# Kernel optimization log

Hardware: AMD Instinct MI355X
Metric: run time of the kernel (lower is better)

Reference implementation:

```python
import jax, jax.numpy as jnp
import numpy as np

B, S, E, H, D = 2, 2048, 1024, 16, 64  # batch, seq(=max_seq_len), embed_dim, heads, atten_dim


def setup_inputs() -> dict:
    key = jax.random.key(0)
    ks = jax.random.split(key, 9)
    s = 0.02
    return {
        "x": jax.random.normal(ks[0], (B, S, E), jnp.float32),
        "Wq": jax.random.normal(ks[1], (H, E, D), jnp.float32) * s,
        "Wk": jax.random.normal(ks[2], (H, E, D), jnp.float32) * s,
        "Wv": jax.random.normal(ks[3], (H, E, D), jnp.float32) * s,
        "bq": jax.random.normal(ks[4], (H, D), jnp.float32) * s,
        "bk": jax.random.normal(ks[5], (H, D), jnp.float32) * s,
        "bv": jax.random.normal(ks[6], (H, D), jnp.float32) * s,
        "Wp": jax.random.normal(ks[7], (H * D, E), jnp.float32) * s,
        "bp": jax.random.normal(ks[8], (E,), jnp.float32) * s,
    }


def reference(x, Wq, Wk, Wv, bq, bk, bv, Wp, bp):
    scale = jnp.sqrt(jnp.float32(D))
    # per-head projections, all heads at once: [B,H,S,D]
    q = jnp.einsum("bse,hed->bhsd", x, Wq) + bq[:, None, :]
    k = jnp.einsum("bse,hed->bhsd", x, Wk) + bk[:, None, :]
    v = jnp.einsum("bse,hed->bhsd", x, Wv) + bv[:, None, :]
    # causal scores [B,H,S,S], additive -inf mask above diagonal (as in the buffer)
    score = jnp.einsum("bhsd,bhtd->bhst", q, k) / scale
    mask = jnp.triu(jnp.full((S, S), -jnp.inf, jnp.float32), k=1)
    score = score + mask
    probs = jax.nn.softmax(score, axis=-1)
    attn = jnp.einsum("bhst,bhtd->bhsd", probs, v)
    # concat heads -> [B,S,H*D], then projection + ReLU
    concat = attn.transpose(0, 2, 1, 3).reshape(B, S, H * D)
    out = jax.nn.relu(concat @ Wp + bp)
    return out
```

## Files before the change

kernel.cpp:

```cpp
#include <hip/hip_runtime.h>

#define S_LEN 2048
#define E_DIM 1024
#define H_NUM 16
#define D_DIM 64

typedef unsigned short u16;
using bf16x8 = __attribute__((ext_vector_type(8))) short;
using f32x4  = __attribute__((ext_vector_type(4))) float;

#define MFMA16(A, B, C) __builtin_amdgcn_mfma_f32_16x16x32_bf16(A, B, C, 0, 0, 0)

__device__ __forceinline__ u16 f2bf(float f) {
    unsigned u = __float_as_uint(f);
    u += 0x7fffu + ((u >> 16) & 1u);
    return (u16)(u >> 16);
}
__device__ __forceinline__ unsigned pack_bf16_tr(float lo, float hi) {
    return (__float_as_uint(lo) >> 16) | (__float_as_uint(hi) & 0xffff0000u);
}
__device__ __forceinline__ float bfu(unsigned u) { return __uint_as_float(u << 16); }
__device__ __forceinline__ f32x4 fzero4() { f32x4 z; z[0]=0.f; z[1]=0.f; z[2]=0.f; z[3]=0.f; return z; }

__device__ __forceinline__ void gll16(const u16* g, u16* l) {
    __builtin_amdgcn_global_load_lds(
        (const __attribute__((address_space(1))) void*)g,
        (__attribute__((address_space(3))) void*)l, 16, 0, 0);
}

__global__ __launch_bounds__(256) void cvt_bf16(const float* __restrict__ in, u16* __restrict__ outp, int n) {
    int i4 = (blockIdx.x * 256 + threadIdx.x) * 4;
    if (i4 < n) {
        float4 f = *(const float4*)(in + i4);
        unsigned lo = (unsigned)f2bf(f.x) | ((unsigned)f2bf(f.y) << 16);
        unsigned hi = (unsigned)f2bf(f.z) | ((unsigned)f2bf(f.w) << 16);
        uint2 p; p.x = lo; p.y = hi;
        *(uint2*)(outp + i4) = p;
    }
}

__device__ __forceinline__ void cvt_t_tile(const float* __restrict__ bin, u16* __restrict__ bout,
                                           int R, int C, int r0, int c0) {
    __shared__ float t[64][65];
    const int tid = threadIdx.x;
    const int lr = tid >> 2, lc = (tid & 3) * 16;

    const float* src = bin + (size_t)(r0 + lr) * C + c0 + lc;
    #pragma unroll
    for (int j = 0; j < 4; j++) {
        float4 f = *(const float4*)(src + j * 4);
        t[lr][lc + j * 4 + 0] = f.x; t[lr][lc + j * 4 + 1] = f.y;
        t[lr][lc + j * 4 + 2] = f.z; t[lr][lc + j * 4 + 3] = f.w;
    }
    __syncthreads();

    u16* dst = bout + (size_t)(c0 + lr) * R + r0 + lc;
    u16 vals[16];
    #pragma unroll
    for (int i = 0; i < 16; i++) vals[i] = f2bf(t[lc + i][lr]);
    uint4 pa, pb;
    pa.x = vals[0] | (vals[1] << 16);  pa.y = vals[2] | (vals[3] << 16);
    pa.z = vals[4] | (vals[5] << 16);  pa.w = vals[6] | (vals[7] << 16);
    pb.x = vals[8] | (vals[9] << 16);  pb.y = vals[10] | (vals[11] << 16);
    pb.z = vals[12] | (vals[13] << 16); pb.w = vals[14] | (vals[15] << 16);
    *(uint4*)dst = pa;
    *(uint4*)(dst + 8) = pb;
}

__global__ __launch_bounds__(256) void cvt_bf16_t(const float* __restrict__ in, u16* __restrict__ outp,
                                                  int R, int C) {
    const float* bin = in + (size_t)blockIdx.z * R * C;
    u16* bout = outp + (size_t)blockIdx.z * R * C;
    cvt_t_tile(bin, bout, R, C, blockIdx.y * 64, blockIdx.x * 64);
}

__global__ __launch_bounds__(256) void cvt_w3_t(
    const float* __restrict__ Wq, const float* __restrict__ Wk, const float* __restrict__ Wv,
    u16* __restrict__ wqt, u16* __restrict__ wkt, u16* __restrict__ wvt) {
    const int which = blockIdx.z >> 4, bh = blockIdx.z & 15;
    const float* in = (which == 0) ? Wq : (which == 1) ? Wk : Wv;
    u16* outp = (which == 0) ? wqt : (which == 1) ? wkt : wvt;
    const float* bin = in + (size_t)bh * E_DIM * D_DIM;
    u16* bout = outp + (size_t)bh * E_DIM * D_DIM;
    cvt_t_tile(bin, bout, E_DIM, D_DIM, blockIdx.y * 64, 0);
}

__global__ __launch_bounds__(256) void vt_prep(const u16* __restrict__ v, u16* __restrict__ vt) {
    const int st = blockIdx.x;
    const int bhi = blockIdx.y;
    __shared__ u16 t[64 * 72];
    const int tid = threadIdx.x;
    const int wave = tid >> 6, lane = tid & 63;

    const u16* src = v + (size_t)bhi * S_LEN * D_DIM + (size_t)(st * 64 + lane) * D_DIM + wave * 16;
    uint4 a = *(const uint4*)(src);
    uint4 b = *(const uint4*)(src + 8);
    unsigned w[8] = { a.x, a.y, a.z, a.w, b.x, b.y, b.z, b.w };
    #pragma unroll
    for (int j = 0; j < 8; j++) {
        t[(wave * 16 + 2 * j    ) * 72 + lane] = (u16)(w[j] & 0xffffu);
        t[(wave * 16 + 2 * j + 1) * 72 + lane] = (u16)(w[j] >> 16);
    }
    __syncthreads();

    const int dr = tid >> 2, sc = (tid & 3) * 16;
    u16* dst = vt + (size_t)bhi * D_DIM * S_LEN + (size_t)dr * S_LEN + st * 64 + sc;
    *(uint4*)(dst    ) = *(const uint4*)(&t[dr * 72 + sc    ]);
    *(uint4*)(dst + 8) = *(const uint4*)(&t[dr * 72 + sc + 8]);
}

__global__ __launch_bounds__(256) void qkv_gemm(
    const u16* __restrict__ xb, const u16* __restrict__ wcat,
    const float* __restrict__ bq, const float* __restrict__ bk, const float* __restrict__ bv,
    u16* __restrict__ oq, u16* __restrict__ okk, u16* __restrict__ ov)
{
    const int m0 = blockIdx.x * 128;
    const int n0 = blockIdx.y * 128;

    __shared__ u16 As[128 * 32];
    __shared__ u16 Bs[128 * 32];

    const int tid  = threadIdx.x;
    const int wave = tid >> 6, lane = tid & 63, quad = lane >> 4, l16 = lane & 15;
    const int mh = wave >> 1, nh = wave & 1;

    const int lrow = lane >> 2, lcol = (lane & 3) * 8;
    const u16* aBase = xb   + (size_t)(m0 + wave * 32 + lrow) * E_DIM + lcol;
    const u16* bBase = wcat + (size_t)(n0 + wave * 32 + lrow) * E_DIM + lcol;
    u16* aLds0 = &As[(wave * 32     ) * 32];
    u16* aLds1 = &As[(wave * 32 + 16) * 32];
    u16* bLds0 = &Bs[(wave * 32     ) * 32];
    u16* bLds1 = &Bs[(wave * 32 + 16) * 32];

    f32x4 acc[4][4];
    #pragma unroll
    for (int j = 0; j < 4; j++)
        #pragma unroll
        for (int mi = 0; mi < 4; mi++) acc[j][mi] = fzero4();

    for (int k0 = 0; k0 < E_DIM; k0 += 32) {
        __syncthreads();
        gll16(aBase + k0,                 aLds0);
        gll16(aBase + k0 + 16 * E_DIM,    aLds1);
        gll16(bBase + k0,                 bLds0);
        gll16(bBase + k0 + 16 * E_DIM,    bLds1);
        __syncthreads();

        bf16x8 af[4];
        #pragma unroll
        for (int mi = 0; mi < 4; mi++)
            af[mi] = *(const bf16x8*)(&As[(mh * 64 + mi * 16 + l16) * 32 + quad * 8]);
        #pragma unroll
        for (int j = 0; j < 4; j++) {
            bf16x8 bfv = *(const bf16x8*)(&Bs[(nh * 64 + j * 16 + l16) * 32 + quad * 8]);
            #pragma unroll
            for (int mi = 0; mi < 4; mi++)
                acc[j][mi] = MFMA16(af[mi], bfv, acc[j][mi]);
        }
    }

    const float QSCL = 0.125f * 1.44269504089f;
    u16* outp[3] = { oq, okk, ov };
    const float* biasp[3] = { bq, bk, bv };
    #pragma unroll
    for (int j = 0; j < 4; j++) {
        const int n = n0 + nh * 64 + j * 16 + l16;
        const int t = n >> 10, h = (n >> 6) & 15, d = n & 63;
        float bia = biasp[t][h * D_DIM + d];
        const float scl = (t == 0) ? QSCL : 1.0f;
        u16* dst = outp[t];
        #pragma unroll
        for (int mi = 0; mi < 4; mi++) {
            #pragma unroll
            for (int r = 0; r < 4; r++) {
                int m = m0 + mh * 64 + mi * 16 + quad * 4 + r;
                int b = m >> 11, s = m & 2047;
                dst[((size_t)(b * H_NUM + h) * S_LEN + s) * D_DIM + d] =
                    f2bf((acc[j][mi][r] + bia) * scl);
            }
        }
    }
}

__global__ __launch_bounds__(256, 4) void attn_split(
    const u16* __restrict__ q, const u16* __restrict__ k, const u16* __restrict__ vt,
    u16* __restrict__ op0, u16* __restrict__ op1,
    float* __restrict__ ls0, float* __restrict__ ls1)
{
    const int x = blockIdx.x;
    const int p = x & 15, half = x >> 4;
    const int h  = blockIdx.y;
    const int bb = blockIdx.z;

    const size_t headoff = (size_t)(bb * H_NUM + h) * S_LEN * D_DIM;
    const u16* qh  = q  + headoff;
    const u16* kh  = k  + headoff;
    const u16* vth = vt + headoff;

    u16*   opart = half ? op1 : op0;
    float* lsum  = half ? ls1 : ls0;

    __shared__ u16 Ks[2][64 * 64];
    __shared__ u16 Vts[2][64 * 64];
    __shared__ u16 QP[64 * 64];

    const int tid  = threadIdx.x;
    const int wave = tid >> 6, lane = tid & 63, quad = lane >> 4, l16 = lane & 15;
    const int srow = tid >> 2, scg = tid & 3;

    const int gr = wave * 8 + (lane >> 3);
    const int gc = lane & 7;
    const int cl = gc ^ (gr & 7);
    const u16* kbase = kh  + (size_t)gr * D_DIM + cl * 8;
    const u16* vbase = vth + (size_t)gr * S_LEN + cl * 8;
    u16* kl0[2] = { &Ks[0][wave * 512], &Ks[1][wave * 512] };
    u16* kl1[2] = { &Ks[0][2048 + wave * 512], &Ks[1][2048 + wave * 512] };
    u16* vl0[2] = { &Vts[0][wave * 512], &Vts[1][wave * 512] };
    u16* vl1[2] = { &Vts[0][2048 + wave * 512], &Vts[1][2048 + wave * 512] };

    const int sx_lo = ((quad    ) ^ (l16 & 7)) * 8;
    const int sx_hi = ((quad + 4) ^ (l16 & 7)) * 8;
    int psw[4];
    #pragma unroll
    for (int nt = 0; nt < 4; nt++)
        psw[nt] = wave * 1024 + l16 * 64 + (((nt * 2 + (quad >> 1)) ^ (l16 & 7)) * 8) + (quad & 1) * 4;

    const int qw = wave * 16 + l16;

    #pragma unroll 1
    for (int seg = 0; seg < 2; seg++) {
        const int qt = seg ? (31 - p) : p;
        const int n  = qt + 1;
        const int r0 = half ? ((n + 1) >> 1) : 0;
        const int r1 = half ? n : ((n + 1) >> 1);
        const int nIt = r1 - r0;

        __syncthreads();
        if (nIt > 0) {
            gll16(kbase + (size_t)r0 * 4096,                       kl0[0]);
            gll16(kbase + (size_t)r0 * 4096 + 2048,                kl1[0]);
            gll16(vbase + (size_t)r0 * 64,                         vl0[0]);
            gll16(vbase + (size_t)r0 * 64 + (size_t)32 * S_LEN,    vl1[0]);
        }

        {
            const u16* qs = qh + (size_t)(qt * 64 + srow) * D_DIM + scg * 16;
            *(uint4*)(&QP[srow * 64 + (((scg * 2    ) ^ (srow & 7)) * 8)]) = *(const uint4*)(qs);
            *(uint4*)(&QP[srow * 64 + (((scg * 2 + 1) ^ (srow & 7)) * 8)]) = *(const uint4*)(qs + 8);
        }
        bf16x8 bq0 = *(const bf16x8*)(&QP[(wave * 16 + l16) * 64 + sx_lo]);
        bf16x8 bq1 = *(const bf16x8*)(&QP[(wave * 16 + l16) * 64 + sx_hi]);

        f32x4 o[4];
        #pragma unroll
        for (int nt = 0; nt < 4; nt++) o[nt] = fzero4();
        float lsv = 0.f;

        const int qg = qt * 64 + qw;

        for (int i = 0; i < nIt; i++) {
            const int kt = r0 + i;
            const u16* ksb = &Ks[i & 1][0];
            const u16* vsb = &Vts[i & 1][0];
            __syncthreads();

            if (i + 1 < nIt) {
                const int nb = (i + 1) & 1;
                gll16(kbase + (size_t)(kt + 1) * 4096,                    kl0[nb]);
                gll16(kbase + (size_t)(kt + 1) * 4096 + 2048,             kl1[nb]);
                gll16(vbase + (size_t)(kt + 1) * 64,                      vl0[nb]);
                gll16(vbase + (size_t)(kt + 1) * 64 + (size_t)32 * S_LEN, vl1[nb]);
            }

            f32x4 st[4];
            #pragma unroll
            for (int nt = 0; nt < 4; nt++) {
                bf16x8 ak0 = *(const bf16x8*)(&ksb[(nt * 16 + l16) * 64 + sx_lo]);
                bf16x8 ak1 = *(const bf16x8*)(&ksb[(nt * 16 + l16) * 64 + sx_hi]);
                st[nt] = fzero4();
                st[nt] = MFMA16(ak0, bq0, st[nt]);
                st[nt] = MFMA16(ak1, bq1, st[nt]);
            }

            #pragma unroll
            for (int nt = 0; nt < 4; nt++) {
                float pe[4];
                if (kt == qt) {
                    #pragma unroll
                    for (int r = 0; r < 4; r++) {
                        int kkg = kt * 64 + nt * 16 + quad * 4 + r;
                        pe[r] = (kkg > qg) ? 0.f : exp2f(st[nt][r]);
                    }
                } else {
                    #pragma unroll
                    for (int r = 0; r < 4; r++) pe[r] = exp2f(st[nt][r]);
                }
                lsv += pe[0] + pe[1] + pe[2] + pe[3];
                uint2 pk;
                pk.x = pack_bf16_tr(pe[0], pe[1]);
                pk.y = pack_bf16_tr(pe[2], pe[3]);
                *(uint2*)(&QP[psw[nt]]) = pk;
            }

            bf16x8 ap0 = *(const bf16x8*)(&QP[wave * 1024 + l16 * 64 + sx_lo]);
            bf16x8 ap1 = *(const bf16x8*)(&QP[wave * 1024 + l16 * 64 + sx_hi]);
            #pragma unroll
            for (int nt = 0; nt < 4; nt++) {
                bf16x8 bv0 = *(const bf16x8*)(&vsb[(nt * 16 + l16) * 64 + sx_lo]);
                bf16x8 bv1 = *(const bf16x8*)(&vsb[(nt * 16 + l16) * 64 + sx_hi]);
                o[nt] = MFMA16(ap0, bv0, o[nt]);
                o[nt] = MFMA16(ap1, bv1, o[nt]);
            }
        }

        lsv += __shfl_xor(lsv, 16); lsv += __shfl_xor(lsv, 32);
        const size_t rowb = (size_t)(bb * H_NUM + h) * S_LEN + qt * 64;
        if (quad == 0) lsum[rowb + wave * 16 + l16] = lsv;
        #pragma unroll
        for (int nt = 0; nt < 4; nt++) {
            #pragma unroll
            for (int r = 0; r < 4; r++) {
                opart[(rowb + wave * 16 + quad * 4 + r) * D_DIM + nt * 16 + l16] =
                    f2bf(o[nt][r]);
            }
        }
    }
}

__global__ __launch_bounds__(256) void out_proj(
    const u16* __restrict__ op0, const u16* __restrict__ op1,
    const float* __restrict__ ls0, const float* __restrict__ ls1,
    const u16* __restrict__ wpt, const float* __restrict__ bp, float* __restrict__ out)
{
    const int m0 = blockIdx.x * 128;
    const int n0 = blockIdx.y * 128;

    __shared__ u16 As[128 * 40];
    __shared__ u16 Bs[128 * 40];

    const int tid  = threadIdx.x;
    const int wave = tid >> 6, lane = tid & 63, quad = lane >> 4, l16 = lane & 15;
    const int mh = wave >> 1, nh = wave & 1;

    const int arow = tid >> 1, acol = (tid & 1) * 16;
    const int m = m0 + arow, bI = m >> 11, sI = m & 2047;
    const size_t oprow0 = (size_t)bI * (H_NUM * S_LEN) + sI;

    float inv[16];
    #pragma unroll
    for (int hh = 0; hh < 16; hh++) {
        size_t r = oprow0 + (size_t)hh * S_LEN;
        inv[hh] = 1.0f / (ls0[r] + ls1[r]);
    }

    const u16* bptr = wpt + (size_t)(n0 + arow) * E_DIM + acol;

    f32x4 acc[4][4];
    #pragma unroll
    for (int j = 0; j < 4; j++)
        #pragma unroll
        for (int mi = 0; mi < 4; mi++) acc[j][mi] = fzero4();

    uint4 a0, a1, c0, c1, pB0, pB1;
    {
        const int e = acol, hh = e >> 6, d0 = e & 63;
        const u16* p0 = op0 + (oprow0 + (size_t)hh * S_LEN) * D_DIM + d0;
        const u16* p1 = op1 + (oprow0 + (size_t)hh * S_LEN) * D_DIM + d0;
        a0 = *(const uint4*)p0; a1 = *(const uint4*)(p0 + 8);
        c0 = *(const uint4*)p1; c1 = *(const uint4*)(p1 + 8);
    }
    pB0 = *(const uint4*)bptr;  pB1 = *(const uint4*)(bptr + 8);

    for (int k0 = 0; k0 < E_DIM; k0 += 32) {
        __syncthreads();
        {
            const int e = k0 + acol, hh = e >> 6;
            const float iv = inv[hh];
            unsigned wa[8] = { a0.x, a0.y, a0.z, a0.w, a1.x, a1.y, a1.z, a1.w };
            unsigned wc[8] = { c0.x, c0.y, c0.z, c0.w, c1.x, c1.y, c1.z, c1.w };
            u16 vals[16];
            #pragma unroll
            for (int j = 0; j < 8; j++) {
                float lo = (bfu(wa[j] & 0xffffu) + bfu(wc[j] & 0xffffu)) * iv;
                float hi = (bfu(wa[j] >> 16)     + bfu(wc[j] >> 16))     * iv;
                vals[2 * j]     = f2bf(lo);
                vals[2 * j + 1] = f2bf(hi);
            }
            uint4 pa, pb;
            pa.x = vals[0] | (vals[1] << 16);   pa.y = vals[2] | (vals[3] << 16);
            pa.z = vals[4] | (vals[5] << 16);   pa.w = vals[6] | (vals[7] << 16);
            pb.x = vals[8] | (vals[9] << 16);   pb.y = vals[10] | (vals[11] << 16);
            pb.z = vals[12] | (vals[13] << 16); pb.w = vals[14] | (vals[15] << 16);
            *(uint4*)(&As[arow * 40 + acol    ]) = pa;
            *(uint4*)(&As[arow * 40 + acol + 8]) = pb;
        }
        *(uint4*)(&Bs[arow * 40 + acol    ]) = pB0;
        *(uint4*)(&Bs[arow * 40 + acol + 8]) = pB1;
        __syncthreads();

        if (k0 + 32 < E_DIM) {
            const int e = k0 + 32 + acol, hh = e >> 6, d0 = e & 63;
            const u16* p0 = op0 + (oprow0 + (size_t)hh * S_LEN) * D_DIM + d0;
            const u16* p1 = op1 + (oprow0 + (size_t)hh * S_LEN) * D_DIM + d0;
            a0 = *(const uint4*)p0; a1 = *(const uint4*)(p0 + 8);
            c0 = *(const uint4*)p1; c1 = *(const uint4*)(p1 + 8);
            pB0 = *(const uint4*)(bptr + k0 + 32);  pB1 = *(const uint4*)(bptr + k0 + 40);
        }

        bf16x8 af[4];
        #pragma unroll
        for (int mi = 0; mi < 4; mi++)
            af[mi] = *(const bf16x8*)(&As[(mh * 64 + mi * 16 + l16) * 40 + quad * 8]);
        #pragma unroll
        for (int j = 0; j < 4; j++) {
            bf16x8 bfv = *(const bf16x8*)(&Bs[(nh * 64 + j * 16 + l16) * 40 + quad * 8]);
            #pragma unroll
            for (int mi = 0; mi < 4; mi++)
                acc[j][mi] = MFMA16(af[mi], bfv, acc[j][mi]);
        }
    }

    #pragma unroll
    for (int j = 0; j < 4; j++) {
        int n = n0 + nh * 64 + j * 16 + l16;
        float bia = bp[n];
        #pragma unroll
        for (int mi = 0; mi < 4; mi++) {
            #pragma unroll
            for (int r = 0; r < 4; r++) {
                int mm = m0 + mh * 64 + mi * 16 + quad * 4 + r;
                out[(size_t)mm * E_DIM + n] = fmaxf(acc[j][mi][r] + bia, 0.f);
            }
        }
    }
}

extern "C" void kernel_launch(void* const* d_in, const int* in_sizes, int n_in,
                              void* d_out, int out_size, void* d_ws, size_t ws_size,
                              hipStream_t stream)
{
    (void)in_sizes; (void)n_in; (void)out_size; (void)ws_size;
    const float* x  = (const float*)d_in[0];
    const float* Wq = (const float*)d_in[1];
    const float* Wk = (const float*)d_in[2];
    const float* Wv = (const float*)d_in[3];
    const float* bq = (const float*)d_in[4];
    const float* bk = (const float*)d_in[5];
    const float* bv = (const float*)d_in[6];
    const float* Wp = (const float*)d_in[7];
    const float* bp = (const float*)d_in[8];
    float* out = (float*)d_out;

    const size_t QKV_ELEMS = (size_t)2 * H_NUM * S_LEN * D_DIM;
    const size_t W_ELEMS   = (size_t)H_NUM * E_DIM * D_DIM;

    u16* q   = (u16*)d_ws;
    u16* k   = q   + QKV_ELEMS;
    u16* v   = k   + QKV_ELEMS;
    u16* op1 = v   + QKV_ELEMS;
    u16* xb  = op1 + QKV_ELEMS;
    u16* wqt = xb  + QKV_ELEMS;
    u16* wkt = wqt + W_ELEMS;
    u16* wvt = wkt + W_ELEMS;
    u16* wpt = wvt + W_ELEMS;
    u16* vtr = xb;
    u16* op0 = v;
    float* ls0 = (float*)wqt;
    float* ls1 = ls0 + (size_t)2 * H_NUM * S_LEN;

    cvt_bf16<<<dim3(4096), 256, 0, stream>>>(x, xb, (int)QKV_ELEMS);
    cvt_w3_t<<<dim3(1, 16, 48), 256, 0, stream>>>(Wq, Wk, Wv, wqt, wkt, wvt);
    cvt_bf16_t<<<dim3(16, 16, 1), 256, 0, stream>>>(Wp, wpt, H_NUM * D_DIM, E_DIM);

    qkv_gemm<<<dim3(32, 24), 256, 0, stream>>>(xb, wqt, bq, bk, bv, q, k, v);
    vt_prep<<<dim3(32, 32), 256, 0, stream>>>(v, vtr);
    attn_split<<<dim3(32, 16, 2), 256, 0, stream>>>(q, k, vtr, op0, op1, ls0, ls1);
    out_proj<<<dim3(32, 8), 256, 0, stream>>>(op0, op1, ls0, ls1, wpt, bp, out);
}
```

Before: 208.0 us.

## Share K/V tiles across paired query tiles and split combine into own kernel

The attention kernel now processes both paired query tiles (p and 31-p) in one pass over the key range, so each K/V tile loaded into shared memory feeds two query tiles while kt is within the short tile's range. The key range is re-split between the two halves to balance work. The normalization and merge of the two partial outputs moves from the out_proj prologue into a separate attn_combine kernel that writes a bf16 concat matrix, and out_proj then streams it directly. This raises register pressure and adds a kernel launch plus an extra round trip through memory.

Result: slower. 321.4 us (+54.5%).

```diff
diff --git a/kernel.cpp b/kernel.cpp
--- a/kernel.cpp
+++ b/kernel.cpp
@@ -189,6 +189,7 @@
 {
     const int x = blockIdx.x;
     const int p = x & 15, half = x >> 4;
+    const int qa = p, qb = 31 - p;
     const int h  = blockIdx.y;
     const int bb = blockIdx.z;
 
@@ -199,6 +200,11 @@
 
     u16*   opart = half ? op1 : op0;
     float* lsum  = half ? ls1 : ls0;
+
+    const int s  = (p <= 7) ? (16 - p) : 8;
+    const int r0 = half ? s : 0;
+    const int r1 = half ? (qb + 1) : s;
+    const int nIt = r1 - r0;
 
     __shared__ u16 Ks[2][64 * 64];
     __shared__ u16 Vts[2][64 * 64];
@@ -225,112 +231,171 @@
     for (int nt = 0; nt < 4; nt++)
         psw[nt] = wave * 1024 + l16 * 64 + (((nt * 2 + (quad >> 1)) ^ (l16 & 7)) * 8) + (quad & 1) * 4;
 
-    const int qw = wave * 16 + l16;
-
-    #pragma unroll 1
-    for (int seg = 0; seg < 2; seg++) {
-        const int qt = seg ? (31 - p) : p;
-        const int n  = qt + 1;
-        const int r0 = half ? ((n + 1) >> 1) : 0;
-        const int r1 = half ? n : ((n + 1) >> 1);
-        const int nIt = r1 - r0;
-
+    gll16(kbase + (size_t)r0 * 4096,                       kl0[0]);
+    gll16(kbase + (size_t)r0 * 4096 + 2048,                kl1[0]);
+    gll16(vbase + (size_t)r0 * 64,                         vl0[0]);
+    gll16(vbase + (size_t)r0 * 64 + (size_t)32 * S_LEN,    vl1[0]);
+
+    bf16x8 bqa0, bqa1, bqb0, bqb1;
+    {
+        const u16* qs = qh + (size_t)(qa * 64 + srow) * D_DIM + scg * 16;
+        *(uint4*)(&QP[srow * 64 + (((scg * 2    ) ^ (srow & 7)) * 8)]) = *(const uint4*)(qs);
+        *(uint4*)(&QP[srow * 64 + (((scg * 2 + 1) ^ (srow & 7)) * 8)]) = *(const uint4*)(qs + 8);
+        bqa0 = *(const bf16x8*)(&QP[(wave * 16 + l16) * 64 + sx_lo]);
+        bqa1 = *(const bf16x8*)(&QP[(wave * 16 + l16) * 64 + sx_hi]);
+    }
+    {
+        const u16* qs = qh + (size_t)(qb * 64 + srow) * D_DIM + scg * 16;
+        *(uint4*)(&QP[srow * 64 + (((scg * 2    ) ^ (srow & 7)) * 8)]) = *(const uint4*)(qs);
+        *(uint4*)(&QP[srow * 64 + (((scg * 2 + 1) ^ (srow & 7)) * 8)]) = *(const uint4*)(qs + 8);
+        bqb0 = *(const bf16x8*)(&QP[(wave * 16 + l16) * 64 + sx_lo]);
+        bqb1 = *(const bf16x8*)(&QP[(wave * 16 + l16) * 64 + sx_hi]);
+    }
+
+    f32x4 oa[4], ob[4];
+    #pragma unroll
+    for (int nt = 0; nt < 4; nt++) { oa[nt] = fzero4(); ob[nt] = fzero4(); }
+    float la = 0.f, lb = 0.f;
+
+    const int qw  = wave * 16 + l16;
+    const int qga = qa * 64 + qw;
+    const int qgb = qb * 64 + qw;
+
+    for (int i = 0; i < nIt; i++) {
+        const int kt = r0 + i;
+        const u16* ksb = &Ks[i & 1][0];
+        const u16* vsb = &Vts[i & 1][0];
         __syncthreads();
-        if (nIt > 0) {
-            gll16(kbase + (size_t)r0 * 4096,                       kl0[0]);
-            gll16(kbase + (size_t)r0 * 4096 + 2048,                kl1[0]);
-            gll16(vbase + (size_t)r0 * 64,                         vl0[0]);
-            gll16(vbase + (size_t)r0 * 64 + (size_t)32 * S_LEN,    vl1[0]);
-        }
-
+
+        if (i + 1 < nIt) {
+            const int nb = (i + 1) & 1;
+            gll16(kbase + (size_t)(kt + 1) * 4096,                    kl0[nb]);
+            gll16(kbase + (size_t)(kt + 1) * 4096 + 2048,             kl1[nb]);
+            gll16(vbase + (size_t)(kt + 1) * 64,                      vl0[nb]);
+            gll16(vbase + (size_t)(kt + 1) * 64 + (size_t)32 * S_LEN, vl1[nb]);
+        }
+
+        const bool both = (kt <= qa);
+
+        f32x4 stb[4], sta[4];
+        #pragma unroll
+        for (int nt = 0; nt < 4; nt++) {
+            bf16x8 ak0 = *(const bf16x8*)(&ksb[(nt * 16 + l16) * 64 + sx_lo]);
+            bf16x8 ak1 = *(const bf16x8*)(&ksb[(nt * 16 + l16) * 64 + sx_hi]);
+            stb[nt] = fzero4();
+            stb[nt] = MFMA16(ak0, bqb0, stb[nt]);
+            stb[nt] = MFMA16(ak1, bqb1, stb[nt]);
+            if (both) {
+                sta[nt] = fzero4();
+                sta[nt] = MFMA16(ak0, bqa0, sta[nt]);
+                sta[nt] = MFMA16(ak1, bqa1, sta[nt]);
+            }
+        }
+
+        bf16x8 apb0, apb1, apa0, apa1;
         {
-            const u16* qs = qh + (size_t)(qt * 64 + srow) * D_DIM + scg * 16;
-            *(uint4*)(&QP[srow * 64 + (((scg * 2    ) ^ (srow & 7)) * 8)]) = *(const uint4*)(qs);
-            *(uint4*)(&QP[srow * 64 + (((scg * 2 + 1) ^ (srow & 7)) * 8)]) = *(const uint4*)(qs + 8);
-        }
-        bf16x8 bq0 = *(const bf16x8*)(&QP[(wave * 16 + l16) * 64 + sx_lo]);
-        bf16x8 bq1 = *(const bf16x8*)(&QP[(wave * 16 + l16) * 64 + sx_hi]);
-
-        f32x4 o[4];
-        #pragma unroll
-        for (int nt = 0; nt < 4; nt++) o[nt] = fzero4();
-        float lsv = 0.f;
-
-        const int qg = qt * 64 + qw;
-
-        for (int i = 0; i < nIt; i++) {
-            const int kt = r0 + i;
-            const u16* ksb = &Ks[i & 1][0];
-            const u16* vsb = &Vts[i & 1][0];
-            __syncthreads();
-
-            if (i + 1 < nIt) {
-                const int nb = (i + 1) & 1;
-                gll16(kbase + (size_t)(kt + 1) * 4096,                    kl0[nb]);
-                gll16(kbase + (size_t)(kt + 1) * 4096 + 2048,             kl1[nb]);
-                gll16(vbase + (size_t)(kt + 1) * 64,                      vl0[nb]);
-                gll16(vbase + (size_t)(kt + 1) * 64 + (size_t)32 * S_LEN, vl1[nb]);
-            }
-
-            f32x4 st[4];
-            #pragma unroll
-            for (int nt = 0; nt < 4; nt++) {
-                bf16x8 ak0 = *(const bf16x8*)(&ksb[(nt * 16 + l16) * 64 + sx_lo]);
-                bf16x8 ak1 = *(const bf16x8*)(&ksb[(nt * 16 + l16) * 64 + sx_hi]);
-                st[nt] = fzero4();
-                st[nt] = MFMA16(ak0, bq0, st[nt]);
-                st[nt] = MFMA16(ak1, bq1, st[nt]);
-            }
-
             #pragma unroll
             for (int nt = 0; nt < 4; nt++) {
                 float pe[4];
-                if (kt == qt) {
+                if (kt == qb) {
                     #pragma unroll
                     for (int r = 0; r < 4; r++) {
                         int kkg = kt * 64 + nt * 16 + quad * 4 + r;
-                        pe[r] = (kkg > qg) ? 0.f : exp2f(st[nt][r]);
+                        pe[r] = (kkg > qgb) ? 0.f : exp2f(stb[nt][r]);
                     }
                 } else {
                     #pragma unroll
-                    for (int r = 0; r < 4; r++) pe[r] = exp2f(st[nt][r]);
+                    for (int r = 0; r < 4; r++) pe[r] = exp2f(stb[nt][r]);
                 }
-                lsv += pe[0] + pe[1] + pe[2] + pe[3];
+                lb += pe[0] + pe[1] + pe[2] + pe[3];
                 uint2 pk;
                 pk.x = pack_bf16_tr(pe[0], pe[1]);
                 pk.y = pack_bf16_tr(pe[2], pe[3]);
                 *(uint2*)(&QP[psw[nt]]) = pk;
             }
-
-            bf16x8 ap0 = *(const bf16x8*)(&QP[wave * 1024 + l16 * 64 + sx_lo]);
-            bf16x8 ap1 = *(const bf16x8*)(&QP[wave * 1024 + l16 * 64 + sx_hi]);
+            apb0 = *(const bf16x8*)(&QP[wave * 1024 + l16 * 64 + sx_lo]);
+            apb1 = *(const bf16x8*)(&QP[wave * 1024 + l16 * 64 + sx_hi]);
+        }
+        if (both) {
             #pragma unroll
             for (int nt = 0; nt < 4; nt++) {
-                bf16x8 bv0 = *(const bf16x8*)(&vsb[(nt * 16 + l16) * 64 + sx_lo]);
-                bf16x8 bv1 = *(const bf16x8*)(&vsb[(nt * 16 + l16) * 64 + sx_hi]);
-                o[nt] = MFMA16(ap0, bv0, o[nt]);
-                o[nt] = MFMA16(ap1, bv1, o[nt]);
+                float pe[4];
+                if (kt == qa) {
+                    #pragma unroll
+                    for (int r = 0; r < 4; r++) {
+                        int kkg = kt * 64 + nt * 16 + quad * 4 + r;
+                        pe[r] = (kkg > qga) ? 0.f : exp2f(sta[nt][r]);
+                    }
+                } else {
+                    #pragma unroll
+                    for (int r = 0; r < 4; r++) pe[r] = exp2f(sta[nt][r]);
+                }
+                la += pe[0] + pe[1] + pe[2] + pe[3];
+                uint2 pk;
+                pk.x = pack_bf16_tr(pe[0], pe[1]);
+                pk.y = pack_bf16_tr(pe[2], pe[3]);
+                *(uint2*)(&QP[psw[nt]]) = pk;
             }
-        }
-
-        lsv += __shfl_xor(lsv, 16); lsv += __shfl_xor(lsv, 32);
-        const size_t rowb = (size_t)(bb * H_NUM + h) * S_LEN + qt * 64;
-        if (quad == 0) lsum[rowb + wave * 16 + l16] = lsv;
+            apa0 = *(const bf16x8*)(&QP[wave * 1024 + l16 * 64 + sx_lo]);
+            apa1 = *(const bf16x8*)(&QP[wave * 1024 + l16 * 64 + sx_hi]);
+        }
+
         #pragma unroll
         for (int nt = 0; nt < 4; nt++) {
-            #pragma unroll
-            for (int r = 0; r < 4; r++) {
-                opart[(rowb + wave * 16 + quad * 4 + r) * D_DIM + nt * 16 + l16] =
-                    f2bf(o[nt][r]);
+            bf16x8 bv0 = *(const bf16x8*)(&vsb[(nt * 16 + l16) * 64 + sx_lo]);
+            bf16x8 bv1 = *(const bf16x8*)(&vsb[(nt * 16 + l16) * 64 + sx_hi]);
+            ob[nt] = MFMA16(apb0, bv0, ob[nt]);
+            ob[nt] = MFMA16(apb1, bv1, ob[nt]);
+            if (both) {
+                oa[nt] = MFMA16(apa0, bv0, oa[nt]);
+                oa[nt] = MFMA16(apa1, bv1, oa[nt]);
             }
         }
     }
-}
-
-__global__ __launch_bounds__(256) void out_proj(
+
+    la += __shfl_xor(la, 16); la += __shfl_xor(la, 32);
+    lb += __shfl_xor(lb, 16); lb += __shfl_xor(lb, 32);
+    const size_t rowa = (size_t)(bb * H_NUM + h) * S_LEN + qa * 64;
+    const size_t rowb = (size_t)(bb * H_NUM + h) * S_LEN + qb * 64;
+    if (quad == 0) {
+        lsum[rowa + wave * 16 + l16] = la;
+        lsum[rowb + wave * 16 + l16] = lb;
+    }
+    #pragma unroll
+    for (int nt = 0; nt < 4; nt++) {
+        #pragma unroll
+        for (int r = 0; r < 4; r++) {
+            opart[(rowa + wave * 16 + quad * 4 + r) * D_DIM + nt * 16 + l16] = f2bf(oa[nt][r]);
+            opart[(rowb + wave * 16 + quad * 4 + r) * D_DIM + nt * 16 + l16] = f2bf(ob[nt][r]);
+        }
+    }
+}
+
+__global__ __launch_bounds__(256) void attn_combine(
     const u16* __restrict__ op0, const u16* __restrict__ op1,
     const float* __restrict__ ls0, const float* __restrict__ ls1,
-    const u16* __restrict__ wpt, const float* __restrict__ bp, float* __restrict__ out)
+    u16* __restrict__ cc)
+{
+    const int idx = blockIdx.x * 256 + threadIdx.x;
+    const int row = idx >> 4;
+    const int d0  = (idx & 15) * 4;
+    const float inv = 1.0f / (ls0[row] + ls1[row]);
+    uint2 a = *(const uint2*)(op0 + (size_t)row * 64 + d0);
+    uint2 b = *(const uint2*)(op1 + (size_t)row * 64 + d0);
+    float o0 = bfu(a.x & 0xffffu) + bfu(b.x & 0xffffu);
+    float o1 = bfu(a.x >> 16)     + bfu(b.x >> 16);
+    float o2 = bfu(a.y & 0xffffu) + bfu(b.y & 0xffffu);
+    float o3 = bfu(a.y >> 16)     + bfu(b.y >> 16);
+    uint2 pk;
+    pk.x = (unsigned)f2bf(o0 * inv) | ((unsigned)f2bf(o1 * inv) << 16);
+    pk.y = (unsigned)f2bf(o2 * inv) | ((unsigned)f2bf(o3 * inv) << 16);
+    const int bbi = row >> 15, hh = (row >> 11) & 15, ss = row & 2047;
+    *(uint2*)(cc + ((size_t)(bbi * S_LEN + ss)) * E_DIM + hh * 64 + d0) = pk;
+}
+
+__global__ __launch_bounds__(256) void out_proj(
+    const u16* __restrict__ concat, const u16* __restrict__ wpt,
+    const float* __restrict__ bp, float* __restrict__ out)
 {
     const int m0 = blockIdx.x * 128;
     const int n0 = blockIdx.y * 128;
@@ -343,16 +408,8 @@
     const int mh = wave >> 1, nh = wave & 1;
 
     const int arow = tid >> 1, acol = (tid & 1) * 16;
-    const int m = m0 + arow, bI = m >> 11, sI = m & 2047;
-    const size_t oprow0 = (size_t)bI * (H_NUM * S_LEN) + sI;
-
-    float inv[16];
-    #pragma unroll
-    for (int hh = 0; hh < 16; hh++) {
-        size_t r = oprow0 + (size_t)hh * S_LEN;
-        inv[hh] = 1.0f / (ls0[r] + ls1[r]);
-    }
-
+
+    const u16* aptr = concat + (size_t)(m0 + arow) * E_DIM + acol;
     const u16* bptr = wpt + (size_t)(n0 + arow) * E_DIM + acol;
 
     f32x4 acc[4][4];
@@ -361,49 +418,20 @@
         #pragma unroll
         for (int mi = 0; mi < 4; mi++) acc[j][mi] = fzero4();
 
-    uint4 a0, a1, c0, c1, pB0, pB1;
-    {
-        const int e = acol, hh = e >> 6, d0 = e & 63;
-        const u16* p0 = op0 + (oprow0 + (size_t)hh * S_LEN) * D_DIM + d0;
-        const u16* p1 = op1 + (oprow0 + (size_t)hh * S_LEN) * D_DIM + d0;
-        a0 = *(const uint4*)p0; a1 = *(const uint4*)(p0 + 8);
-        c0 = *(const uint4*)p1; c1 = *(const uint4*)(p1 + 8);
-    }
-    pB0 = *(const uint4*)bptr;  pB1 = *(const uint4*)(bptr + 8);
+    uint4 pA0, pA1, pB0, pB1;
+    pA0 = *(const uint4*)(aptr);     pA1 = *(const uint4*)(aptr + 8);
+    pB0 = *(const uint4*)(bptr);     pB1 = *(const uint4*)(bptr + 8);
 
     for (int k0 = 0; k0 < E_DIM; k0 += 32) {
         __syncthreads();
-        {
-            const int e = k0 + acol, hh = e >> 6;
-            const float iv = inv[hh];
-            unsigned wa[8] = { a0.x, a0.y, a0.z, a0.w, a1.x, a1.y, a1.z, a1.w };
-            unsigned wc[8] = { c0.x, c0.y, c0.z, c0.w, c1.x, c1.y, c1.z, c1.w };
-            u16 vals[16];
-            #pragma unroll
-            for (int j = 0; j < 8; j++) {
-                float lo = (bfu(wa[j] & 0xffffu) + bfu(wc[j] & 0xffffu)) * iv;
-                float hi = (bfu(wa[j] >> 16)     + bfu(wc[j] >> 16))     * iv;
-                vals[2 * j]     = f2bf(lo);
-                vals[2 * j + 1] = f2bf(hi);
-            }
-            uint4 pa, pb;
-            pa.x = vals[0] | (vals[1] << 16);   pa.y = vals[2] | (vals[3] << 16);
-            pa.z = vals[4] | (vals[5] << 16);   pa.w = vals[6] | (vals[7] << 16);
-            pb.x = vals[8] | (vals[9] << 16);   pb.y = vals[10] | (vals[11] << 16);
-            pb.z = vals[12] | (vals[13] << 16); pb.w = vals[14] | (vals[15] << 16);
-            *(uint4*)(&As[arow * 40 + acol    ]) = pa;
-            *(uint4*)(&As[arow * 40 + acol + 8]) = pb;
-        }
+        *(uint4*)(&As[arow * 40 + acol    ]) = pA0;
+        *(uint4*)(&As[arow * 40 + acol + 8]) = pA1;
         *(uint4*)(&Bs[arow * 40 + acol    ]) = pB0;
         *(uint4*)(&Bs[arow * 40 + acol + 8]) = pB1;
         __syncthreads();
 
         if (k0 + 32 < E_DIM) {
-            const int e = k0 + 32 + acol, hh = e >> 6, d0 = e & 63;
-            const u16* p0 = op0 + (oprow0 + (size_t)hh * S_LEN) * D_DIM + d0;
-            const u16* p1 = op1 + (oprow0 + (size_t)hh * S_LEN) * D_DIM + d0;
-            a0 = *(const uint4*)p0; a1 = *(const uint4*)(p0 + 8);
-            c0 = *(const uint4*)p1; c1 = *(const uint4*)(p1 + 8);
+            pA0 = *(const uint4*)(aptr + k0 + 32);  pA1 = *(const uint4*)(aptr + k0 + 40);
             pB0 = *(const uint4*)(bptr + k0 + 32);  pB1 = *(const uint4*)(bptr + k0 + 40);
         }
 
@@ -428,8 +456,8 @@
         for (int mi = 0; mi < 4; mi++) {
             #pragma unroll
             for (int r = 0; r < 4; r++) {
-                int mm = m0 + mh * 64 + mi * 16 + quad * 4 + r;
-                out[(size_t)mm * E_DIM + n] = fmaxf(acc[j][mi][r] + bia, 0.f);
+                int m = m0 + mh * 64 + mi * 16 + quad * 4 + r;
+                out[(size_t)m * E_DIM + n] = fmaxf(acc[j][mi][r] + bia, 0.f);
             }
         }
     }
@@ -465,6 +493,7 @@
     u16* wpt = wvt + W_ELEMS;
     u16* vtr = xb;
     u16* op0 = v;
+    u16* cc  = q;
     float* ls0 = (float*)wqt;
     float* ls1 = ls0 + (size_t)2 * H_NUM * S_LEN;
 
@@ -475,5 +504,6 @@
     qkv_gemm<<<dim3(32, 24), 256, 0, stream>>>(xb, wqt, bq, bk, bv, q, k, v);
     vt_prep<<<dim3(32, 32), 256, 0, stream>>>(v, vtr);
     attn_split<<<dim3(32, 16, 2), 256, 0, stream>>>(q, k, vtr, op0, op1, ls0, ls1);
-    out_proj<<<dim3(32, 8), 256, 0, stream>>>(op0, op1, ls0, ls1, wpt, bp, out);
-}
+    attn_combine<<<dim3(4096), 256, 0, stream>>>(op0, op1, ls0, ls1, cc);
+    out_proj<<<dim3(32, 8), 256, 0, stream>>>(cc, wpt, bp, out);
+}
```
